# Kernel optimization log

Measured on AMD Instinct MI355X. Metric: run time of the kernel, lower is better.

The kernel has to match this reference:

```python
import jax, jax.numpy as jnp
import numpy as np
from jax import lax

# SLAYER SRMALPHA neuron / simulation constants (from init params)
THETA = 10.0      # spike threshold
TAU_SR = 10.0     # synaptic (PSP) alpha-kernel time constant
TAU_REF = 1.0     # refractory alpha-kernel time constant
SCALE_REF = 2.0   # refractory kernel scale (x theta)
TS = 1.0          # simulation timestep


def _alpha_filter(x, tau):
    """Causal convolution of x[T, ...] with the SLAYER alpha kernel
    k[n] = (n*TS/tau) * exp(1 - n*TS/tau)  (note k[0] = 0),
    implemented as a 2-state linear recurrence (exact, O(T)).
    k[n] = c * n * a**n with a = exp(-TS/tau), c = e*TS/tau.
    """
    a = jnp.asarray(np.exp(-TS / tau), x.dtype)
    c = jnp.asarray(np.e * TS / tau, x.dtype)

    def step(carry, xn):
        p, q = carry              # p[n-1] = sum a^{n-1-m} x[m]; q[n-1] = sum (n-1-m) a^{n-1-m} x[m]
        q = a * q + a * p         # q[n]
        p = a * p + xn            # p[n]
        return (p, q), c * q      # y[n] = c*q[n]  (x[n] has weight k[0]=0)

    z = jnp.zeros_like(x[0])
    _, y = lax.scan(step, (z, z), x)
    return y


def _spike_with_refractory(u):
    """SLAYER spike: threshold membrane potential u[T, B, O]; each emitted
    spike injects the refractory alpha kernel -scaleRef*theta*(t/tauRef)*exp(1-t/tauRef)
    into the future membrane potential. Same 2-state alpha recurrence, but the
    filtered signal is the (data-dependent) spike train -> sequential scan.
    """
    a = jnp.asarray(np.exp(-TS / TAU_REF), u.dtype)
    c = jnp.asarray(-SCALE_REF * THETA * np.e * TS / TAU_REF, u.dtype)

    def step(carry, un):
        p, q = carry
        q = a * q + a * p                       # refractory trace of past spikes
        s = (un + c * q >= THETA).astype(un.dtype)
        p = a * p + s
        return (p, q), s

    z = jnp.zeros_like(u[0])
    _, s = lax.scan(step, (z, z), u)
    return s


def setup_inputs() -> dict:
    key = jax.random.key(0)
    k1, k2 = jax.random.split(key)
    B, CIN, COUT, T = 32, 1024, 1024, 500
    spike_input = (jax.random.uniform(k1, (B, CIN, 1, 1, T)) < 0.05).astype(jnp.float32)
    W = jax.random.normal(k2, (COUT, CIN), dtype=jnp.float32) * (1.0 / np.sqrt(CIN))
    return {"spike_input": spike_input, "W": W}


def reference(spike_input, W):
    B, C, _, _, T = spike_input.shape
    O = W.shape[0]
    x = spike_input.reshape(B, C, T).transpose(2, 0, 1)   # [T, B, C]
    psp = _alpha_filter(x, TAU_SR)                        # temporal PSP filter
    u = jnp.einsum('tbc,oc->tbo', psp, W)                 # slayer.dense = 1x1 conv = GEMM
    s = _spike_with_refractory(u)                         # threshold + refractory
    return s.transpose(1, 2, 0).reshape(B, O, 1, 1, T)
```

## Files before the change

### kernel.cpp

```cpp
#include <hip/hip_runtime.h>
#include <cstddef>
#include <cstdint>

#define T_DIM 500
#define B_DIM 32
#define C_DIM 1024
#define O_DIM 1024
#define M_DIM (T_DIM * B_DIM)
#define MP_DIM 16128
#define BO_DIM (B_DIM * O_DIM)

typedef __attribute__((ext_vector_type(8))) short bf16x8;
typedef __attribute__((ext_vector_type(4))) float f32x4;

static __device__ __forceinline__ ushort f2bf(float x) {
  unsigned u = __float_as_uint(x);
  return (ushort)((u + 0x7FFF + ((u >> 16) & 1)) >> 16);
}
static __device__ __forceinline__ float bf2f(ushort u) {
  return __uint_as_float(((unsigned)u) << 16);
}

static __device__ __forceinline__ bf16x8 ldsr(const ushort* p) {
  bf16x8 d;
  asm volatile("ds_read_b128 %0, %1"
               : "=v"(d)
               : "v"((unsigned)(uintptr_t)(const __attribute__((address_space(3))) ushort*)p));
  return d;
}

__global__ __launch_bounds__(256) void k_transpose(const float* __restrict__ x,
                                                   ushort* __restrict__ xt) {
  __shared__ float tile[32][33];
  const int b  = blockIdx.z;
  const int t0 = blockIdx.x * 32;
  const int c0 = blockIdx.y * 32;
  const int tx = threadIdx.x;
  const int ty = threadIdx.y;

  const int t = t0 + tx;
  if (t < T_DIM) {
#pragma unroll
    for (int r = 0; r < 4; ++r) {
      const int c = c0 + ty + r * 8;
      tile[ty + r * 8][tx] = x[((size_t)b * C_DIM + c) * T_DIM + t];
    }
  }
  __syncthreads();
#pragma unroll
  for (int r = 0; r < 4; ++r) {
    const int tt = t0 + ty + r * 8;
    if (tt < T_DIM) {
      xt[((size_t)tt * B_DIM + b) * C_DIM + c0 + tx] = f2bf(tile[tx][ty + r * 8]);
    }
  }
}

__global__ __launch_bounds__(256) void k_cast_w(const float4* __restrict__ W,
                                                ushort* __restrict__ Wb) {
  const int i = blockIdx.x * 256 + threadIdx.x;
  const float4 w = W[i];
  ushort* o = Wb + (size_t)i * 4;
  o[0] = f2bf(w.x); o[1] = f2bf(w.y); o[2] = f2bf(w.z); o[3] = f2bf(w.w);
}

__global__ __launch_bounds__(512, 4) void k_gemm_bf16(const ushort* __restrict__ A,
                                                      const ushort* __restrict__ Bw,
                                                      ushort* __restrict__ C) {
  __shared__ ushort lds[24576];

  const int tid  = threadIdx.x;
  const int wid  = tid >> 6;
  const int lane = tid & 63;

  const int orig = blockIdx.x;
  const int swz  = (orig & 7) * 63 + (orig >> 3);
  const int row0 = (swz >> 3) * 256;
  const int col0 = (swz & 7) * 128;

  const int wm = wid >> 1;
  const int wn = wid & 1;

  f32x4 acc[4][4] = {};

  const int srow = tid >> 2;
  const int sk   = ((tid & 3) * 8) ^ (((tid >> 5) & 1) << 4);
  const ushort* Abase = A  + (size_t)(row0 + srow) * C_DIM + sk;
  const ushort* Bbase = Bw + (size_t)(col0 + srow) * C_DIM + sk;

  const int fr  = lane & 15;
  const int fko = ((lane >> 4) * 8) ^ (((lane >> 3) & 1) << 4);
  const int aoff = (wm * 64 + fr) * 32 + fko;
  const int boff = 8192 + (wn * 64 + fr) * 32 + fko;

#define STAGE_A(K0S, SB)                                                          \
  _Pragma("unroll")                                                               \
  for (int rh = 0; rh < 2; ++rh)                                                  \
    __builtin_amdgcn_global_load_lds(                                             \
        (const __attribute__((address_space(1))) void*)(Abase + (size_t)rh * 128 * C_DIM + (K0S)), \
        (__attribute__((address_space(3))) void*)&lds[(SB) + rh * 4096 + wid * 512], 16, 0, 0)

#define STAGE_B(K0S, SB)                                                          \
  __builtin_amdgcn_global_load_lds(                                               \
      (const __attribute__((address_space(1))) void*)(Bbase + (K0S)),             \
      (__attribute__((address_space(3))) void*)&lds[(SB) + 8192 + wid * 512], 16, 0, 0)

  STAGE_A(0, 0);
  STAGE_B(0, 0);
  STAGE_A(32, 12288);
  STAGE_B(32, 12288);

  for (int t = 0; t < 32; ++t) {
    const int sb = (t & 1) * 12288;
    bf16x8 a[4], b[4];

    if (t < 31) { asm volatile("s_waitcnt vmcnt(3)" ::: "memory"); }
    else        { asm volatile("s_waitcnt vmcnt(0)" ::: "memory"); }
    __builtin_amdgcn_s_barrier();

#pragma unroll
    for (int i = 0; i < 4; ++i) a[i] = ldsr(&lds[sb + aoff + i * 512]);
#pragma unroll
    for (int j = 0; j < 4; ++j) b[j] = ldsr(&lds[sb + boff + j * 512]);
    asm volatile("s_waitcnt lgkmcnt(0)" ::: "memory");
    __builtin_amdgcn_sched_barrier(0);
    __builtin_amdgcn_s_barrier();

    if (t < 30) {
      STAGE_A((t + 2) * 32, sb);
      STAGE_B((t + 2) * 32, sb);
    }

    __builtin_amdgcn_s_setprio(1);
#pragma unroll
    for (int i = 0; i < 4; ++i)
#pragma unroll
      for (int j = 0; j < 4; ++j)
        acc[i][j] = __builtin_amdgcn_mfma_f32_16x16x32_bf16(a[i], b[j], acc[i][j], 0, 0, 0);
    __builtin_amdgcn_s_setprio(0);
  }

  const int crow = (lane >> 4) * 4;
  const int ccol = lane & 15;
#pragma unroll
  for (int i = 0; i < 4; ++i)
#pragma unroll
    for (int j = 0; j < 4; ++j) {
      ushort* cp = C + (size_t)(row0 + wm * 64 + i * 16 + crow) * O_DIM
                     + (col0 + wn * 64 + j * 16 + ccol);
#pragma unroll
      for (int r = 0; r < 4; ++r) cp[(size_t)r * O_DIM] = f2bf(acc[i][j][r]);
    }
#undef STAGE_A
#undef STAGE_B
}

__global__ __launch_bounds__(64) void k_scan(const ushort* __restrict__ v,
                                             float* __restrict__ out) {
  const int g = blockIdx.x * 64 + threadIdx.x;

  const float a1 = 0.90483741803595952f;
  const float c1 = 0.27182818284590452f;
  const float a2 = 0.36787944117144233f;
  const float c2 = -54.365636569180905f;

  float p1 = 0.f, q1 = 0.f;
  float p2 = 0.f, q2 = 0.f;

  const ushort* vp = v + g;
  float* op = out + (size_t)g * T_DIM;

  constexpr int D  = 20;
  constexpr int NC = 25;

  ushort b0[D], b1[D], b2[D];
#pragma unroll
  for (int j = 0; j < D; ++j) b0[j] = vp[(size_t)j * BO_DIM];
#pragma unroll
  for (int j = 0; j < D; ++j) b1[j] = vp[(size_t)(D + j) * BO_DIM];
#pragma unroll
  for (int j = 0; j < D; ++j) b2[j] = vp[(size_t)(2 * D + j) * BO_DIM];

#pragma unroll 5
  for (int c = 0; c < NC; ++c) {
    const int cn = (c + 3 < NC) ? (c + 3) : (NC - 1);
    ushort bn[D];
    {
      const size_t base = (size_t)cn * D;
#pragma unroll
      for (int j = 0; j < D; ++j) bn[j] = vp[(base + j) * BO_DIM];
    }

    float rr[D];
#pragma unroll
    for (int j = 0; j < D; ++j) {
      const float vn = bf2f(b0[j]);
      q1 = a1 * q1 + a1 * p1;
      p1 = a1 * p1 + vn;
      const float u = c1 * q1;
      q2 = a2 * q2 + a2 * p2;
      const float s = (u + c2 * q2 >= 10.0f) ? 1.0f : 0.0f;
      p2 = a2 * p2 + s;
      rr[j] = s;
    }

    float* o = op + c * D;
#pragma unroll
    for (int j = 0; j < D; j += 4)
      *(float4*)&o[j] = make_float4(rr[j], rr[j + 1], rr[j + 2], rr[j + 3]);

#pragma unroll
    for (int j = 0; j < D; ++j) { b0[j] = b1[j]; b1[j] = b2[j]; b2[j] = bn[j]; }
  }
}

extern "C" void kernel_launch(void* const* d_in, const int* in_sizes, int n_in,
                              void* d_out, int out_size, void* d_ws, size_t ws_size,
                              hipStream_t stream) {
  const float* x = (const float*)d_in[0];
  const float* W = (const float*)d_in[1];
  float* out = (float*)d_out;

  ushort* v  = (ushort*)d_ws;
  ushort* xt = v + (size_t)MP_DIM * O_DIM;
  ushort* Wb = xt + (size_t)MP_DIM * C_DIM;

  dim3 g0((T_DIM + 31) / 32, C_DIM / 32, B_DIM);
  k_transpose<<<g0, dim3(32, 8), 0, stream>>>(x, xt);

  k_cast_w<<<(O_DIM * C_DIM / 4) / 256, 256, 0, stream>>>((const float4*)W, Wb);

  k_gemm_bf16<<<(MP_DIM / 256) * (O_DIM / 128), 512, 0, stream>>>(xt, Wb, v);

  k_scan<<<BO_DIM / 64, 64, 0, stream>>>(v, out);
}
```

Baseline: 89.58 us.

## Enlarge GEMM tile to 256x256 with K=64 stages and interleaved ping-pong pipeline

The bf16 GEMM moves from 256x128 output tiles with K=32 stages to 256x256 tiles with K=64 stages held in a 128 KB double-buffered LDS. Each iteration now splits into quarter-tile MFMA phases with barriers between them, so global-to-LDS loads for the next tile are spread across the compute phases. The block-to-XCD mapping is also rebalanced for the new grid of 252 blocks. The aim is higher arithmetic intensity per LDS byte and less global traffic per flop. The cost is fewer blocks, more accumulator registers (occupancy bound cut from 4 to 2) and many more barriers.

```diff
diff --git a/kernel.cpp b/kernel.cpp
--- a/kernel.cpp
+++ b/kernel.cpp
@@ -64,95 +64,132 @@
   o[0] = f2bf(w.x); o[1] = f2bf(w.y); o[2] = f2bf(w.z); o[3] = f2bf(w.w);
 }
 
-__global__ __launch_bounds__(512, 4) void k_gemm_bf16(const ushort* __restrict__ A,
+__global__ __launch_bounds__(512, 2) void k_gemm_bf16(const ushort* __restrict__ A,
                                                       const ushort* __restrict__ Bw,
                                                       ushort* __restrict__ C) {
-  __shared__ ushort lds[24576];
+  __shared__ ushort lds[65536];
 
   const int tid  = threadIdx.x;
   const int wid  = tid >> 6;
   const int lane = tid & 63;
 
   const int orig = blockIdx.x;
-  const int swz  = (orig & 7) * 63 + (orig >> 3);
-  const int row0 = (swz >> 3) * 256;
-  const int col0 = (swz & 7) * 128;
-
-  const int wm = wid >> 1;
-  const int wn = wid & 1;
-
-  f32x4 acc[4][4] = {};
-
-  const int srow = tid >> 2;
-  const int sk   = ((tid & 3) * 8) ^ (((tid >> 5) & 1) << 4);
-  const ushort* Abase = A  + (size_t)(row0 + srow) * C_DIM + sk;
-  const ushort* Bbase = Bw + (size_t)(col0 + srow) * C_DIM + sk;
-
-  const int fr  = lane & 15;
-  const int fko = ((lane >> 4) * 8) ^ (((lane >> 3) & 1) << 4);
-  const int aoff = (wm * 64 + fr) * 32 + fko;
-  const int boff = 8192 + (wn * 64 + fr) * 32 + fko;
-
-#define STAGE_A(K0S, SB)                                                          \
-  _Pragma("unroll")                                                               \
-  for (int rh = 0; rh < 2; ++rh)                                                  \
-    __builtin_amdgcn_global_load_lds(                                             \
-        (const __attribute__((address_space(1))) void*)(Abase + (size_t)rh * 128 * C_DIM + (K0S)), \
-        (__attribute__((address_space(3))) void*)&lds[(SB) + rh * 4096 + wid * 512], 16, 0, 0)
-
-#define STAGE_B(K0S, SB)                                                          \
-  __builtin_amdgcn_global_load_lds(                                               \
-      (const __attribute__((address_space(1))) void*)(Bbase + (K0S)),             \
-      (__attribute__((address_space(3))) void*)&lds[(SB) + 8192 + wid * 512], 16, 0, 0)
-
-  STAGE_A(0, 0);
-  STAGE_B(0, 0);
-  STAGE_A(32, 12288);
-  STAGE_B(32, 12288);
-
-  for (int t = 0; t < 32; ++t) {
-    const int sb = (t & 1) * 12288;
-    bf16x8 a[4], b[4];
-
-    if (t < 31) { asm volatile("s_waitcnt vmcnt(3)" ::: "memory"); }
+  const int xcd  = orig & 7;
+  const int basq = (xcd < 4) ? xcd * 32 : 128 + (xcd - 4) * 31;
+  const int wgid = basq + (orig >> 3);
+  const int row0 = (wgid >> 2) * 256;
+  const int col0 = (wgid & 3) * 256;
+
+  const int wm = wid >> 2;
+  const int wn = wid & 3;
+  const int bh  = wn >> 1;
+  const int br0 = (wn & 1) * 64;
+
+  f32x4 acc[8][4] = {};
+
+  const int sk = ((tid & 7) * 8) ^ (((tid >> 6) & 1) << 4);
+  const ushort* Ab = A  + (size_t)(row0 + (tid >> 3)) * C_DIM + sk;
+  const ushort* Bb = Bw + (size_t)(col0 + (tid >> 3)) * C_DIM + sk;
+
+  const int fr = lane & 15;
+  const int fk = ((lane >> 4) * 8) ^ (((lane >> 3) & 1) << 4);
+
+#define STG(SRC, MATOFF, TILE, HALF, SLOT)                                     \
+  _Pragma("unroll")                                                            \
+  for (int L = 0; L < 2; ++L)                                                  \
+    __builtin_amdgcn_global_load_lds(                                          \
+        (const __attribute__((address_space(1))) void*)((SRC) + (size_t)((HALF) * 128 + L * 64) * C_DIM + (TILE) * 64), \
+        (__attribute__((address_space(3))) void*)&lds[(SLOT) + (MATOFF) + (HALF) * 8192 + L * 4096 + tid * 8], 16, 0, 0)
+
+#define RD_A(dst, SLOT, QH)                                                    \
+  _Pragma("unroll")                                                            \
+  for (int i = 0; i < 4; ++i)                                                  \
+    _Pragma("unroll")                                                          \
+    for (int ks = 0; ks < 2; ++ks)                                             \
+      dst[i][ks] = ldsr(&lds[(SLOT) + wm * 8192 + ((QH) * 64 + i * 16 + fr) * 64 + ks * 32 + fk])
+
+#define RD_B(dst, SLOT, QN)                                                    \
+  _Pragma("unroll")                                                            \
+  for (int jj = 0; jj < 2; ++jj)                                               \
+    _Pragma("unroll")                                                          \
+    for (int ks = 0; ks < 2; ++ks)                                             \
+      dst[jj][ks] = ldsr(&lds[(SLOT) + 16384 + bh * 8192 + (br0 + (QN) * 32 + jj * 16 + fr) * 64 + ks * 32 + fk])
+
+#define MM(QH, QN, Aa, Bv)                                                     \
+  _Pragma("unroll")                                                            \
+  for (int ks = 0; ks < 2; ++ks)                                               \
+    _Pragma("unroll")                                                          \
+    for (int i = 0; i < 4; ++i)                                                \
+      _Pragma("unroll")                                                        \
+      for (int jj = 0; jj < 2; ++jj)                                           \
+        acc[(QH) * 4 + i][(QN) * 2 + jj] = __builtin_amdgcn_mfma_f32_16x16x32_bf16( \
+            Aa[i][ks], Bv[jj][ks], acc[(QH) * 4 + i][(QN) * 2 + jj], 0, 0, 0)
+
+#define LGKM0 do { asm volatile("s_waitcnt lgkmcnt(0)" ::: "memory"); \
+                   __builtin_amdgcn_sched_barrier(0); } while (0)
+#define BAR   __builtin_amdgcn_s_barrier()
+#define PRIO1 __builtin_amdgcn_s_setprio(1)
+#define PRIO0 __builtin_amdgcn_s_setprio(0)
+
+  STG(Ab, 0, 0, 0, 0);      STG(Ab, 0, 0, 1, 0);
+  STG(Bb, 16384, 0, 0, 0);  STG(Bb, 16384, 0, 1, 0);
+  STG(Ab, 0, 1, 0, 32768);  STG(Ab, 0, 1, 1, 32768);
+  asm volatile("s_waitcnt vmcnt(4)" ::: "memory");
+  BAR;
+
+  for (int it = 0; it < 8; ++it) {
+    const int t1 = 2 * it + 1, t2 = 2 * it + 2, t3 = 2 * it + 3;
+    bf16x8 aE0[4][2], aE1[4][2], bE0[2][2], bE1[2][2];
+    bf16x8 aO0[4][2], aO1[4][2], bO0[2][2], bO1[2][2];
+
+    RD_A(aE0, 0, 0); RD_B(bE0, 0, 0);
+    STG(Bb, 16384, t1, 0, 32768);
+    BAR; LGKM0; PRIO1; MM(0, 0, aE0, bE0); PRIO0; BAR;
+    RD_A(aE1, 0, 1);
+    STG(Bb, 16384, t1, 1, 32768);
+    BAR; LGKM0; PRIO1; MM(1, 0, aE1, bE0); PRIO0; BAR;
+    RD_B(bE1, 0, 1);
+    if (it < 7) { STG(Ab, 0, t2, 0, 0); }
+    BAR; LGKM0; PRIO1; MM(0, 1, aE0, bE1); PRIO0; BAR;
+    if (it < 7) { STG(Ab, 0, t2, 1, 0); }
+    PRIO1; MM(1, 1, aE1, bE1); PRIO0;
+    if (it < 7) { asm volatile("s_waitcnt vmcnt(4)" ::: "memory"); }
     else        { asm volatile("s_waitcnt vmcnt(0)" ::: "memory"); }
-    __builtin_amdgcn_s_barrier();
-
-#pragma unroll
-    for (int i = 0; i < 4; ++i) a[i] = ldsr(&lds[sb + aoff + i * 512]);
-#pragma unroll
-    for (int j = 0; j < 4; ++j) b[j] = ldsr(&lds[sb + boff + j * 512]);
-    asm volatile("s_waitcnt lgkmcnt(0)" ::: "memory");
-    __builtin_amdgcn_sched_barrier(0);
-    __builtin_amdgcn_s_barrier();
-
-    if (t < 30) {
-      STAGE_A((t + 2) * 32, sb);
-      STAGE_B((t + 2) * 32, sb);
-    }
-
-    __builtin_amdgcn_s_setprio(1);
-#pragma unroll
-    for (int i = 0; i < 4; ++i)
-#pragma unroll
-      for (int j = 0; j < 4; ++j)
-        acc[i][j] = __builtin_amdgcn_mfma_f32_16x16x32_bf16(a[i], b[j], acc[i][j], 0, 0, 0);
-    __builtin_amdgcn_s_setprio(0);
+    BAR;
+    RD_A(aO0, 32768, 0); RD_B(bO0, 32768, 0);
+    if (it < 7) { STG(Bb, 16384, t2, 0, 0); }
+    BAR; LGKM0; PRIO1; MM(0, 0, aO0, bO0); PRIO0; BAR;
+    RD_A(aO1, 32768, 1);
+    if (it < 7) { STG(Bb, 16384, t2, 1, 0); }
+    BAR; LGKM0; PRIO1; MM(1, 0, aO1, bO0); PRIO0; BAR;
+    RD_B(bO1, 32768, 1);
+    if (it < 7) { STG(Ab, 0, t3, 0, 32768); }
+    BAR; LGKM0; PRIO1; MM(0, 1, aO0, bO1); PRIO0; BAR;
+    if (it < 7) { STG(Ab, 0, t3, 1, 32768); }
+    PRIO1; MM(1, 1, aO1, bO1); PRIO0;
+    if (it < 7) { asm volatile("s_waitcnt vmcnt(4)" ::: "memory"); }
+    BAR;
   }
 
   const int crow = (lane >> 4) * 4;
   const int ccol = lane & 15;
 #pragma unroll
-  for (int i = 0; i < 4; ++i)
+  for (int i = 0; i < 8; ++i)
 #pragma unroll
     for (int j = 0; j < 4; ++j) {
-      ushort* cp = C + (size_t)(row0 + wm * 64 + i * 16 + crow) * O_DIM
+      ushort* cp = C + (size_t)(row0 + wm * 128 + i * 16 + crow) * O_DIM
                      + (col0 + wn * 64 + j * 16 + ccol);
 #pragma unroll
       for (int r = 0; r < 4; ++r) cp[(size_t)r * O_DIM] = f2bf(acc[i][j][r]);
     }
-#undef STAGE_A
-#undef STAGE_B
+#undef STG
+#undef RD_A
+#undef RD_B
+#undef MM
+#undef LGKM0
+#undef BAR
+#undef PRIO1
+#undef PRIO0
 }
 
 __global__ __launch_bounds__(64) void k_scan(const ushort* __restrict__ v,
@@ -230,7 +267,7 @@
 
   k_cast_w<<<(O_DIM * C_DIM / 4) / 256, 256, 0, stream>>>((const float4*)W, Wb);
 
-  k_gemm_bf16<<<(MP_DIM / 256) * (O_DIM / 128), 512, 0, stream>>>(xt, Wb, v);
+  k_gemm_bf16<<<(MP_DIM / 256) * (O_DIM / 256), 512, 0, stream>>>(xt, Wb, v);
 
   k_scan<<<BO_DIM / 64, 64, 0, stream>>>(v, out);
 }
```

Result: slower. 102.1 us (+14.0%).

## Use 4-wave GEMM blocks with triple-buffered LDS and single barrier per k-step

Applied to the files above, without the earlier changes.

The GEMM block drops from 8 waves to 4, and each wave now computes a 128x64 tile (8x4 MFMA accumulators) instead of 64x64. LDS grows to three stages, so the next-next tile can be issued right after the LDS fragment reads, removing the second barrier per iteration. The aim is more MFMA work per LDS read and less synchronisation. In exchange it uses more registers per thread and fewer waves per CU, which may reduce the ability to hide latency.

```diff
diff --git a/kernel.cpp b/kernel.cpp
--- a/kernel.cpp
+++ b/kernel.cpp
@@ -64,10 +64,10 @@
   o[0] = f2bf(w.x); o[1] = f2bf(w.y); o[2] = f2bf(w.z); o[3] = f2bf(w.w);
 }
 
-__global__ __launch_bounds__(512, 4) void k_gemm_bf16(const ushort* __restrict__ A,
+__global__ __launch_bounds__(256, 2) void k_gemm_bf16(const ushort* __restrict__ A,
                                                       const ushort* __restrict__ Bw,
                                                       ushort* __restrict__ C) {
-  __shared__ ushort lds[24576];
+  __shared__ ushort lds[36864];
 
   const int tid  = threadIdx.x;
   const int wid  = tid >> 6;
@@ -81,78 +81,77 @@
   const int wm = wid >> 1;
   const int wn = wid & 1;
 
-  f32x4 acc[4][4] = {};
+  f32x4 acc[8][4] = {};
 
   const int srow = tid >> 2;
   const int sk   = ((tid & 3) * 8) ^ (((tid >> 5) & 1) << 4);
-  const ushort* Abase = A  + (size_t)(row0 + srow) * C_DIM + sk;
-  const ushort* Bbase = Bw + (size_t)(col0 + srow) * C_DIM + sk;
+  const ushort* Ab = A  + (size_t)(row0 + srow) * C_DIM + sk;
+  const ushort* Bb = Bw + (size_t)(col0 + srow) * C_DIM + sk;
 
   const int fr  = lane & 15;
   const int fko = ((lane >> 4) * 8) ^ (((lane >> 3) & 1) << 4);
-  const int aoff = (wm * 64 + fr) * 32 + fko;
+  const int aoff = (wm * 128 + fr) * 32 + fko;
   const int boff = 8192 + (wn * 64 + fr) * 32 + fko;
 
-#define STAGE_A(K0S, SB)                                                          \
-  _Pragma("unroll")                                                               \
-  for (int rh = 0; rh < 2; ++rh)                                                  \
-    __builtin_amdgcn_global_load_lds(                                             \
-        (const __attribute__((address_space(1))) void*)(Abase + (size_t)rh * 128 * C_DIM + (K0S)), \
-        (__attribute__((address_space(3))) void*)&lds[(SB) + rh * 4096 + wid * 512], 16, 0, 0)
-
-#define STAGE_B(K0S, SB)                                                          \
-  __builtin_amdgcn_global_load_lds(                                               \
-      (const __attribute__((address_space(1))) void*)(Bbase + (K0S)),             \
-      (__attribute__((address_space(3))) void*)&lds[(SB) + 8192 + wid * 512], 16, 0, 0)
-
-  STAGE_A(0, 0);
-  STAGE_B(0, 0);
-  STAGE_A(32, 12288);
-  STAGE_B(32, 12288);
+#define STG(K0S, SB)                                                              \
+  do {                                                                            \
+    _Pragma("unroll")                                                             \
+    for (int L = 0; L < 4; ++L)                                                   \
+      __builtin_amdgcn_global_load_lds(                                           \
+          (const __attribute__((address_space(1))) void*)(Ab + (size_t)L * 64 * C_DIM + (K0S)), \
+          (__attribute__((address_space(3))) void*)&lds[(SB) + L * 2048 + tid * 8], 16, 0, 0);  \
+    _Pragma("unroll")                                                             \
+    for (int L = 0; L < 2; ++L)                                                   \
+      __builtin_amdgcn_global_load_lds(                                           \
+          (const __attribute__((address_space(1))) void*)(Bb + (size_t)L * 64 * C_DIM + (K0S)), \
+          (__attribute__((address_space(3))) void*)&lds[(SB) + 8192 + L * 2048 + tid * 8], 16, 0, 0); \
+  } while (0)
+
+  STG(0, 0);
+  STG(32, 12288);
+
+  int cur = 0;
+  int nxt = 24576;
 
   for (int t = 0; t < 32; ++t) {
-    const int sb = (t & 1) * 12288;
-    bf16x8 a[4], b[4];
-
-    if (t < 31) { asm volatile("s_waitcnt vmcnt(3)" ::: "memory"); }
+    if (t < 31) { asm volatile("s_waitcnt vmcnt(6)" ::: "memory"); }
     else        { asm volatile("s_waitcnt vmcnt(0)" ::: "memory"); }
     __builtin_amdgcn_s_barrier();
 
-#pragma unroll
-    for (int i = 0; i < 4; ++i) a[i] = ldsr(&lds[sb + aoff + i * 512]);
-#pragma unroll
-    for (int j = 0; j < 4; ++j) b[j] = ldsr(&lds[sb + boff + j * 512]);
+    bf16x8 a[8], b[4];
+#pragma unroll
+    for (int i = 0; i < 8; ++i) a[i] = ldsr(&lds[cur + aoff + i * 512]);
+#pragma unroll
+    for (int j = 0; j < 4; ++j) b[j] = ldsr(&lds[cur + boff + j * 512]);
+
+    if (t <= 29) { STG((t + 2) * 32, nxt); }
+
     asm volatile("s_waitcnt lgkmcnt(0)" ::: "memory");
     __builtin_amdgcn_sched_barrier(0);
-    __builtin_amdgcn_s_barrier();
-
-    if (t < 30) {
-      STAGE_A((t + 2) * 32, sb);
-      STAGE_B((t + 2) * 32, sb);
-    }
-
     __builtin_amdgcn_s_setprio(1);
 #pragma unroll
-    for (int i = 0; i < 4; ++i)
+    for (int i = 0; i < 8; ++i)
 #pragma unroll
       for (int j = 0; j < 4; ++j)
         acc[i][j] = __builtin_amdgcn_mfma_f32_16x16x32_bf16(a[i], b[j], acc[i][j], 0, 0, 0);
     __builtin_amdgcn_s_setprio(0);
+
+    cur = (cur == 24576) ? 0 : cur + 12288;
+    nxt = (nxt == 24576) ? 0 : nxt + 12288;
   }
 
   const int crow = (lane >> 4) * 4;
   const int ccol = lane & 15;
 #pragma unroll
-  for (int i = 0; i < 4; ++i)
+  for (int i = 0; i < 8; ++i)
 #pragma unroll
     for (int j = 0; j < 4; ++j) {
-      ushort* cp = C + (size_t)(row0 + wm * 64 + i * 16 + crow) * O_DIM
+      ushort* cp = C + (size_t)(row0 + wm * 128 + i * 16 + crow) * O_DIM
                      + (col0 + wn * 64 + j * 16 + ccol);
 #pragma unroll
       for (int r = 0; r < 4; ++r) cp[(size_t)r * O_DIM] = f2bf(acc[i][j][r]);
     }
-#undef STAGE_A
-#undef STAGE_B
+#undef STG
 }
 
 __global__ __launch_bounds__(64) void k_scan(const ushort* __restrict__ v,
@@ -230,7 +229,7 @@
 
   k_cast_w<<<(O_DIM * C_DIM / 4) / 256, 256, 0, stream>>>((const float4*)W, Wb);
 
-  k_gemm_bf16<<<(MP_DIM / 256) * (O_DIM / 128), 512, 0, stream>>>(xt, Wb, v);
+  k_gemm_bf16<<<(MP_DIM / 256) * (O_DIM / 128), 256, 0, stream>>>(xt, Wb, v);
 
   k_scan<<<BO_DIM / 64, 64, 0, stream>>>(v, out);
 }
```

Result: no change. 89.95 us (+0.4%).
